# Optimization experiments

Hardware: AMD Instinct MI355X
Metric: run time of the kernel (lower is better)

Reference implementation:

```python
import jax, jax.numpy as jnp
import numpy as np

B, S, D, H = 2, 2048, 1024, 16
DK = D // H


def setup_inputs() -> dict:
    key = jax.random.key(0)
    ks = jax.random.split(key, 12)
    q = jax.random.normal(ks[0], (B, S, D), dtype=jnp.float32)
    k = jax.random.normal(ks[1], (B, S, D), dtype=jnp.float32)
    v = jax.random.normal(ks[2], (B, S, D), dtype=jnp.float32)
    # causal mask: positions where mask == 0 are masked out
    mask = jnp.tril(jnp.ones((S, S), dtype=jnp.int32))[None, None, :, :]
    s = 1.0 / np.sqrt(D)
    Wq = jax.random.uniform(ks[3], (D, D), jnp.float32, -s, s)
    bq = jax.random.uniform(ks[4], (D,), jnp.float32, -s, s)
    Wk = jax.random.uniform(ks[5], (D, D), jnp.float32, -s, s)
    bk = jax.random.uniform(ks[6], (D,), jnp.float32, -s, s)
    Wv = jax.random.uniform(ks[7], (D, D), jnp.float32, -s, s)
    bv = jax.random.uniform(ks[8], (D,), jnp.float32, -s, s)
    Wo = jax.random.uniform(ks[9], (D, D), jnp.float32, -s, s)
    bo = jax.random.uniform(ks[10], (D,), jnp.float32, -s, s)
    return {"q": q, "k": k, "v": v, "mask": mask,
            "Wq": Wq, "bq": bq, "Wk": Wk, "bk": bk,
            "Wv": Wv, "bv": bv, "Wo": Wo, "bo": bo}


def reference(q, k, v, mask, Wq, bq, Wk, bk, Wv, bv, Wo, bo):
    b = q.shape[0]
    # linear projections (nn.Linear: x @ W.T + b), split into heads -> [b,h,s,dk]
    qh = (q @ Wq.T + bq).reshape(b, -1, H, DK).transpose(0, 2, 1, 3)
    kh = (k @ Wk.T + bk).reshape(b, -1, H, DK).transpose(0, 2, 1, 3)
    vh = (v @ Wv.T + bv).reshape(b, -1, H, DK).transpose(0, 2, 1, 3)
    scores = jnp.einsum('bhqd,bhkd->bhqk', qh, kh) / jnp.sqrt(jnp.float32(DK))
    scores = jnp.where(mask == 0, jnp.float32(-1e9), scores)
    attn = jax.nn.softmax(scores, axis=-1)  # dropout p=0.0 -> identity
    out = jnp.einsum('bhqk,bhkd->bhqd', attn, vh)
    out = out.transpose(0, 2, 1, 3).reshape(b, -1, D)
    return out @ Wo.T + bo
```

## Files before the change

kernel.cpp:

```cpp
#include <hip/hip_runtime.h>


typedef _Float16 f16;
typedef __attribute__((ext_vector_type(4))) float   f32x4;
typedef __attribute__((ext_vector_type(8))) _Float16 f16x8;

#define DEVI __device__ __forceinline__

static constexpr int S  = 2048;
static constexpr int D  = 1024;
static constexpr int KK = 1024;
static constexpr int M  = 4096;

DEVI void gload_lds16(const void* g, void* l) {
  __builtin_amdgcn_global_load_lds((const __attribute__((address_space(1))) void*)g,
                                   (__attribute__((address_space(3))) void*)l, 16, 0, 0);
}

DEVI f32x4 mfma16(f16x8 a, f16x8 b, f32x4 c) {
  return __builtin_amdgcn_mfma_f32_16x16x32_f16(a, b, c, 0, 0, 0);
}

DEVI int xorv(int row) { return ((row ^ (row >> 3)) & 7) << 4; }

__global__ __launch_bounds__(256) void cvt_kernel(const float* __restrict__ s0,
                                                  const float* __restrict__ s1,
                                                  const float* __restrict__ s2,
                                                  const float* __restrict__ s3,
                                                  f16* __restrict__ dst, int nper) {
  const float* s = blockIdx.y == 0 ? s0 : blockIdx.y == 1 ? s1 : blockIdx.y == 2 ? s2 : s3;
  f16* d = dst + (size_t)blockIdx.y * nper;
  const int i = (blockIdx.x * 256 + threadIdx.x) * 8;
  f32x4 a = *(const f32x4*)(s + i);
  f32x4 b = *(const f32x4*)(s + i + 4);
  f16x8 r;
#pragma unroll
  for (int j = 0; j < 4; ++j) { r[j] = (f16)a[j]; r[4 + j] = (f16)b[j]; }
  *(f16x8*)(d + i) = r;
}

DEVI void gemm_mainloop(const f16* __restrict__ A, const f16* __restrict__ W,
                        int m0, int n0, f16* As, f16* Bs, f32x4 acc[4][4]) {
  const int tid  = threadIdx.x;
  const int wid  = tid >> 6;
  const int lane = tid & 63;
  const int wr = wid >> 1, wc = wid & 1;

  const f32x4 z4 = {0.f, 0.f, 0.f, 0.f};
#pragma unroll
  for (int mi = 0; mi < 4; ++mi)
#pragma unroll
    for (int ni = 0; ni < 4; ++ni) acc[mi][ni] = z4;

  const int r0 = tid >> 2, c0 = (tid & 3) * 8;
  const int r1 = 64 + r0;
  const f16* Ag0 = A + (size_t)(m0 + r0) * KK + c0;
  const f16* Ag1 = A + (size_t)(m0 + r1) * KK + c0;
  const f16* Bg0 = W + (size_t)(n0 + r0) * KK + c0;
  const f16* Bg1 = W + (size_t)(n0 + r1) * KK + c0;
  f16* As0 = As + wid * 512;
  f16* As1 = As + 2048 + wid * 512;
  f16* Bs0 = Bs + wid * 512;
  f16* Bs1 = Bs + 2048 + wid * 512;

  const int arow = wr * 64 + (lane & 15);
  const int brow = wc * 64 + (lane & 15);
  const int ko   = (lane >> 4) * 8;

  for (int k0 = 0; k0 < KK; k0 += 32) {
    gload_lds16(Ag0 + k0, As0);
    gload_lds16(Ag1 + k0, As1);
    gload_lds16(Bg0 + k0, Bs0);
    gload_lds16(Bg1 + k0, Bs1);
    __syncthreads();
    f16x8 af[4], bf[4];
#pragma unroll
    for (int mi = 0; mi < 4; ++mi) af[mi] = *(const f16x8*)&As[(arow + mi * 16) * 32 + ko];
#pragma unroll
    for (int ni = 0; ni < 4; ++ni) bf[ni] = *(const f16x8*)&Bs[(brow + ni * 16) * 32 + ko];
#pragma unroll
    for (int mi = 0; mi < 4; ++mi)
#pragma unroll
      for (int ni = 0; ni < 4; ++ni)
        acc[mi][ni] = mfma16(af[mi], bf[ni], acc[mi][ni]);
    __syncthreads();
  }
}

__global__ __launch_bounds__(256, 2) void gemm_qkv_kernel(const f16* __restrict__ X,
                                                          const f16* __restrict__ Wp,
                                                          const float* __restrict__ b0,
                                                          const float* __restrict__ b1,
                                                          const float* __restrict__ b2,
                                                          f16* __restrict__ Hd) {
  __shared__ f16 As[128 * 32];
  __shared__ f16 Bs[128 * 32];
  const int z = blockIdx.z;
  const f16* A = X + (size_t)z * (M * KK);
  const f16* W = Wp + (size_t)z * (D * KK);
  const float* bias = z == 0 ? b0 : z == 1 ? b1 : b2;
  f16* dst = Hd + (size_t)z * (size_t)4194304;
  const float scale = (z == 0) ? 0.125f : 1.0f;
  const int m0 = blockIdx.y * 128, n0 = blockIdx.x * 128;

  f32x4 acc[4][4];
  gemm_mainloop(A, W, m0, n0, As, Bs, acc);

  const int lane = threadIdx.x & 63, wid = threadIdx.x >> 6;
  const int wr = wid >> 1, wc = wid & 1;
#pragma unroll
  for (int ni = 0; ni < 4; ++ni) {
    const int col = n0 + wc * 64 + ni * 16 + (lane & 15);
    const float bv = bias[col];
    const int h = col >> 6, dk = col & 63;
#pragma unroll
    for (int mi = 0; mi < 4; ++mi) {
#pragma unroll
      for (int r = 0; r < 4; ++r) {
        const int row = m0 + wr * 64 + mi * 16 + (lane >> 4) * 4 + r;
        const int bb = row >> 11, ss = row & 2047;
        dst[(size_t)((bb * 16 + h) * 2048 + ss) * 64 + dk] = (f16)((acc[mi][ni][r] + bv) * scale);
      }
    }
  }
}

__global__ __launch_bounds__(256, 2) void gemm_out_kernel(const f16* __restrict__ A,
                                                          const f16* __restrict__ W,
                                                          const float* __restrict__ bias,
                                                          float* __restrict__ out) {
  __shared__ f16 As[128 * 32];
  __shared__ f16 Bs[128 * 32];
  const int m0 = blockIdx.y * 128, n0 = blockIdx.x * 128;
  f32x4 acc[4][4];
  gemm_mainloop(A, W, m0, n0, As, Bs, acc);
  const int lane = threadIdx.x & 63, wid = threadIdx.x >> 6;
  const int wr = wid >> 1, wc = wid & 1;
#pragma unroll
  for (int ni = 0; ni < 4; ++ni) {
    const int col = n0 + wc * 64 + ni * 16 + (lane & 15);
    const float bv = bias[col];
#pragma unroll
    for (int mi = 0; mi < 4; ++mi) {
#pragma unroll
      for (int r = 0; r < 4; ++r) {
        const int row = m0 + wr * 64 + mi * 16 + (lane >> 4) * 4 + r;
        out[(size_t)row * 1024 + col] = acc[mi][ni][r] + bv;
      }
    }
  }
}

__global__ __launch_bounds__(256) void vtr_kernel(const f16* __restrict__ Vh,
                                                  f16* __restrict__ VhT) {
  __shared__ f16 T[64][72];
  const int bh = blockIdx.y;
  const int s0 = blockIdx.x * 64;
  const size_t base = (size_t)bh * (S * 64);
  const int tid = threadIdx.x;
#pragma unroll
  for (int i = 0; i < 2; ++i) {
    const int c = i * 256 + tid;
    const int sr = c >> 3, sc = (c & 7) * 8;
    f16x8 v = *(const f16x8*)&Vh[base + (size_t)(s0 + sr) * 64 + sc];
    *(f16x8*)&T[sr][sc] = v;
  }
  __syncthreads();
#pragma unroll
  for (int i = 0; i < 2; ++i) {
    const int c = i * 256 + tid;
    const int dk = c >> 3, so = (c & 7) * 8;
    f16x8 r;
#pragma unroll
    for (int j = 0; j < 8; ++j) r[j] = T[so + j][dk];
    *(f16x8*)&VhT[base + (size_t)dk * S + s0 + so] = r;
  }
}

__global__ __launch_bounds__(256, 2) void attn_kernel(const f16* __restrict__ Qh,
                                                      const f16* __restrict__ Kh,
                                                      const f16* __restrict__ VhT,
                                                      f16* __restrict__ Ao) {
  __shared__ f16 Ks[2][64 * 64];
  __shared__ f16 Vt[2][64 * 64];
  __shared__ f16 Ps[4][32 * 64];

  const int tid = threadIdx.x, wid = tid >> 6, lane = tid & 63;
  const int bh = blockIdx.y;
  const int q0 = (15 - (int)blockIdx.x) * 128;
  const int qw = q0 + wid * 32;
  const size_t base = (size_t)bh * (S * 64);

  const int srow0 = tid >> 3;
  const int scol0 = (((tid & 7) * 16) ^ xorv(srow0)) >> 1;
  const int srow1 = (256 + tid) >> 3;
  const int scol1 = (((tid & 7) * 16) ^ xorv(srow1)) >> 1;
  const int ldsoff0 = wid * 64 * 16;
  const int ldsoff1 = (256 + wid * 64) * 16;

  f16x8 aq[2][2];
#pragma unroll
  for (int mi = 0; mi < 2; ++mi)
#pragma unroll
    for (int ks = 0; ks < 2; ++ks)
      aq[mi][ks] = *(const f16x8*)&Qh[base + (size_t)(qw + mi * 16 + (lane & 15)) * 64 +
                                      ks * 32 + (lane >> 4) * 8];

  const f32x4 z4 = {0.f, 0.f, 0.f, 0.f};
  f32x4 o[2][4];
  float mrow[2][4], lrow[2][4];
#pragma unroll
  for (int mi = 0; mi < 2; ++mi)
#pragma unroll
    for (int r = 0; r < 4; ++r) { mrow[mi][r] = -1e30f; lrow[mi][r] = 0.f; }
#pragma unroll
  for (int mi = 0; mi < 2; ++mi)
#pragma unroll
    for (int dj = 0; dj < 4; ++dj) o[mi][dj] = z4;

  const int ntiles = q0 / 64 + 2;

  {
    const int kv0 = 0;
    gload_lds16(Kh + base + (size_t)(kv0 + srow0) * 64 + scol0, (char*)Ks[0] + ldsoff0);
    gload_lds16(VhT + base + (size_t)srow0 * S + kv0 + scol0,   (char*)Vt[0] + ldsoff0);
    gload_lds16(Kh + base + (size_t)(kv0 + srow1) * 64 + scol1, (char*)Ks[0] + ldsoff1);
    gload_lds16(VhT + base + (size_t)srow1 * S + kv0 + scol1,   (char*)Vt[0] + ldsoff1);
  }

  int cur = 0;
  for (int t = 0; t < ntiles; ++t) {
    const int kv0 = t * 64;
    if (t + 1 < ntiles) {
      const int kn = kv0 + 64;
      f16* Kd = Ks[cur ^ 1];
      f16* Vd = Vt[cur ^ 1];
      gload_lds16(Kh + base + (size_t)(kn + srow0) * 64 + scol0, (char*)Kd + ldsoff0);
      gload_lds16(VhT + base + (size_t)srow0 * S + kn + scol0,   (char*)Vd + ldsoff0);
      gload_lds16(Kh + base + (size_t)(kn + srow1) * 64 + scol1, (char*)Kd + ldsoff1);
      gload_lds16(VhT + base + (size_t)srow1 * S + kn + scol1,   (char*)Vd + ldsoff1);
      asm volatile("s_waitcnt vmcnt(4)" ::: "memory");
    } else {
      asm volatile("s_waitcnt vmcnt(0)" ::: "memory");
    }
    __builtin_amdgcn_sched_barrier(0);
    __builtin_amdgcn_s_barrier();
    __builtin_amdgcn_sched_barrier(0);

    const f16* Kc = Ks[cur];
    const f16* Vc = Vt[cur];

    if (kv0 <= qw + 31) {
      f32x4 sc[2][4];
#pragma unroll
      for (int mi = 0; mi < 2; ++mi)
#pragma unroll
        for (int nj = 0; nj < 4; ++nj) sc[mi][nj] = z4;
      __builtin_amdgcn_s_setprio(1);
#pragma unroll
      for (int nj = 0; nj < 4; ++nj) {
        const int krow = nj * 16 + (lane & 15);
#pragma unroll
        for (int ks = 0; ks < 2; ++ks) {
          f16x8 bk = *(const f16x8*)((const char*)Kc + krow * 128 +
                                     ((ks * 64 + (lane >> 4) * 16) ^ xorv(krow)));
          sc[0][nj] = mfma16(aq[0][ks], bk, sc[0][nj]);
          sc[1][nj] = mfma16(aq[1][ks], bk, sc[1][nj]);
        }
      }
      __builtin_amdgcn_s_setprio(0);
      if (kv0 + 63 > qw) {
#pragma unroll
        for (int mi = 0; mi < 2; ++mi)
#pragma unroll
          for (int nj = 0; nj < 4; ++nj)
#pragma unroll
            for (int r = 0; r < 4; ++r) {
              const int qq = qw + mi * 16 + (lane >> 4) * 4 + r;
              const int kv = kv0 + nj * 16 + (lane & 15);
              if (kv > qq) sc[mi][nj][r] = -1e30f;
            }
      }
      float mnew[2][4], scl[2][4], psum[2][4];
#pragma unroll
      for (int mi = 0; mi < 2; ++mi)
#pragma unroll
        for (int r = 0; r < 4; ++r) {
          float mx = fmaxf(fmaxf(sc[mi][0][r], sc[mi][1][r]), fmaxf(sc[mi][2][r], sc[mi][3][r]));
#pragma unroll
          for (int off = 1; off < 16; off <<= 1) mx = fmaxf(mx, __shfl_xor(mx, off));
          const float mn = fmaxf(mrow[mi][r], mx);
          mnew[mi][r] = mn;
          scl[mi][r]  = exp2f((mrow[mi][r] - mn) * 1.44269504f);
          psum[mi][r] = 0.f;
        }
#pragma unroll
      for (int mi = 0; mi < 2; ++mi)
#pragma unroll
        for (int nj = 0; nj < 4; ++nj) {
#pragma unroll
          for (int r = 0; r < 4; ++r) {
            const float p = exp2f((sc[mi][nj][r] - mnew[mi][r]) * 1.44269504f);
            psum[mi][r] += p;
            const int ql = mi * 16 + (lane >> 4) * 4 + r;
            const int kvl = nj * 16 + (lane & 15);
            *(f16*)((char*)Ps[wid] + ql * 128 + ((kvl * 2) ^ xorv(ql))) = (f16)p;
          }
        }
#pragma unroll
      for (int mi = 0; mi < 2; ++mi)
#pragma unroll
        for (int r = 0; r < 4; ++r) {
          float ps = psum[mi][r];
#pragma unroll
          for (int off = 1; off < 16; off <<= 1) ps += __shfl_xor(ps, off);
          lrow[mi][r] = lrow[mi][r] * scl[mi][r] + ps;
          mrow[mi][r] = mnew[mi][r];
        }
#pragma unroll
      for (int mi = 0; mi < 2; ++mi)
#pragma unroll
        for (int dj = 0; dj < 4; ++dj)
#pragma unroll
          for (int r = 0; r < 4; ++r) o[mi][dj][r] *= scl[mi][r];
      __builtin_amdgcn_s_setprio(1);
#pragma unroll
      for (int ks = 0; ks < 2; ++ks) {
        f16x8 pa[2];
#pragma unroll
        for (int mi = 0; mi < 2; ++mi) {
          const int ql = mi * 16 + (lane & 15);
          pa[mi] = *(const f16x8*)((char*)Ps[wid] + ql * 128 +
                                   ((ks * 64 + (lane >> 4) * 16) ^ xorv(ql)));
        }
#pragma unroll
        for (int dj = 0; dj < 4; ++dj) {
          const int dr = dj * 16 + (lane & 15);
          f16x8 bv = *(const f16x8*)((const char*)Vc + dr * 128 +
                                     ((ks * 64 + (lane >> 4) * 16) ^ xorv(dr)));
          o[0][dj] = mfma16(pa[0], bv, o[0][dj]);
          o[1][dj] = mfma16(pa[1], bv, o[1][dj]);
        }
      }
      __builtin_amdgcn_s_setprio(0);
    }

    __builtin_amdgcn_sched_barrier(0);
    __builtin_amdgcn_s_barrier();
    cur ^= 1;
  }

  const int bb = bh >> 4, hh = bh & 15;
#pragma unroll
  for (int mi = 0; mi < 2; ++mi)
#pragma unroll
    for (int r = 0; r < 4; ++r) {
      const float inv = 1.0f / lrow[mi][r];
      const int qq = qw + mi * 16 + (lane >> 4) * 4 + r;
#pragma unroll
      for (int dj = 0; dj < 4; ++dj) {
        const int dk = dj * 16 + (lane & 15);
        Ao[(size_t)(bb * 2048 + qq) * 1024 + hh * 64 + dk] = (f16)(o[mi][dj][r] * inv);
      }
    }
}

extern "C" void kernel_launch(void* const* d_in, const int* in_sizes, int n_in,
                              void* d_out, int out_size, void* d_ws, size_t ws_size,
                              hipStream_t stream) {
  const float* q  = (const float*)d_in[0];
  const float* k  = (const float*)d_in[1];
  const float* v  = (const float*)d_in[2];
  const float* Wq = (const float*)d_in[4];  const float* bq = (const float*)d_in[5];
  const float* Wk = (const float*)d_in[6];  const float* bk = (const float*)d_in[7];
  const float* Wv = (const float*)d_in[8];  const float* bv = (const float*)d_in[9];
  const float* Wo = (const float*)d_in[10]; const float* bo = (const float*)d_in[11];
  float* out = (float*)d_out;

  char* ws = (char*)d_ws;
  f16* xb = (f16*)(ws);
  f16* wb = (f16*)(ws + 25165824);
  f16* hb = (f16*)(ws + 33554432);
  f16* ao = (f16*)(ws + 58720256);
  f16* vt = (f16*)(ws);

  cvt_kernel<<<dim3(2048, 3), 256, 0, stream>>>(q, k, v, nullptr, xb, 4194304);
  cvt_kernel<<<dim3(512, 4), 256, 0, stream>>>(Wq, Wk, Wv, Wo, wb, 1048576);
  gemm_qkv_kernel<<<dim3(8, 32, 3), 256, 0, stream>>>(xb, wb, bq, bk, bv, hb);
  vtr_kernel<<<dim3(32, 32), 256, 0, stream>>>(hb + 8388608, vt);
  attn_kernel<<<dim3(16, 32), 256, 0, stream>>>(hb, hb + 4194304, vt, ao);
  gemm_out_kernel<<<dim3(8, 32), 256, 0, stream>>>(ao, wb + 3 * 1048576, bo, out);
}
```

Before: 319.6 us.

## Split attention KV range across two blocks and merge with combine kernel

Each query block's causal KV range is split into two halves handled by separate blocks (grid z=2), so twice as many blocks run and per-block work is more balanced. Each half writes an unnormalized fp16 partial output plus running max and sum, and a new combine kernel rescales and merges the two halves into the final attention output. Launch bounds are raised to 3 blocks per SM to fit more occupancy. The cost is extra global traffic for the partials, an extra kernel launch, and fp16 storage of unnormalized accumulators, which could lose precision or overflow.

```diff
diff --git a/kernel.cpp b/kernel.cpp
--- a/kernel.cpp
+++ b/kernel.cpp
@@ -177,19 +177,24 @@
   }
 }
 
-__global__ __launch_bounds__(256, 2) void attn_kernel(const f16* __restrict__ Qh,
+__global__ __launch_bounds__(256, 3) void attn_kernel(const f16* __restrict__ Qh,
                                                       const f16* __restrict__ Kh,
                                                       const f16* __restrict__ VhT,
-                                                      f16* __restrict__ Ao) {
+                                                      f16* __restrict__ pO,
+                                                      float2* __restrict__ ml) {
   __shared__ f16 Ks[2][64 * 64];
   __shared__ f16 Vt[2][64 * 64];
   __shared__ f16 Ps[4][32 * 64];
 
   const int tid = threadIdx.x, wid = tid >> 6, lane = tid & 63;
   const int bh = blockIdx.y;
+  const int z  = blockIdx.z;
   const int q0 = (15 - (int)blockIdx.x) * 128;
   const int qw = q0 + wid * 32;
   const size_t base = (size_t)bh * (S * 64);
+
+  const int half = q0 / 128 + 1;
+  const int t0 = z * half, t1 = t0 + half;
 
   const int srow0 = tid >> 3;
   const int scol0 = (((tid & 7) * 16) ^ xorv(srow0)) >> 1;
@@ -218,10 +223,8 @@
 #pragma unroll
     for (int dj = 0; dj < 4; ++dj) o[mi][dj] = z4;
 
-  const int ntiles = q0 / 64 + 2;
-
   {
-    const int kv0 = 0;
+    const int kv0 = t0 * 64;
     gload_lds16(Kh + base + (size_t)(kv0 + srow0) * 64 + scol0, (char*)Ks[0] + ldsoff0);
     gload_lds16(VhT + base + (size_t)srow0 * S + kv0 + scol0,   (char*)Vt[0] + ldsoff0);
     gload_lds16(Kh + base + (size_t)(kv0 + srow1) * 64 + scol1, (char*)Ks[0] + ldsoff1);
@@ -229,9 +232,9 @@
   }
 
   int cur = 0;
-  for (int t = 0; t < ntiles; ++t) {
+  for (int t = t0; t < t1; ++t) {
     const int kv0 = t * 64;
-    if (t + 1 < ntiles) {
+    if (t + 1 < t1) {
       const int kn = kv0 + 64;
       f16* Kd = Ks[cur ^ 1];
       f16* Vd = Vt[cur ^ 1];
@@ -297,7 +300,7 @@
 #pragma unroll
       for (int mi = 0; mi < 2; ++mi)
 #pragma unroll
-        for (int nj = 0; nj < 4; ++nj) {
+      for (int nj = 0; nj < 4; ++nj) {
 #pragma unroll
           for (int r = 0; r < 4; ++r) {
             const float p = exp2f((sc[mi][nj][r] - mnew[mi][r]) * 1.44269504f);
@@ -350,19 +353,52 @@
     cur ^= 1;
   }
 
-  const int bb = bh >> 4, hh = bh & 15;
+  f16* po = pO + (size_t)z * 4194304 + (size_t)bh * 2048 * 64;
 #pragma unroll
   for (int mi = 0; mi < 2; ++mi)
 #pragma unroll
     for (int r = 0; r < 4; ++r) {
-      const float inv = 1.0f / lrow[mi][r];
       const int qq = qw + mi * 16 + (lane >> 4) * 4 + r;
 #pragma unroll
       for (int dj = 0; dj < 4; ++dj) {
         const int dk = dj * 16 + (lane & 15);
-        Ao[(size_t)(bb * 2048 + qq) * 1024 + hh * 64 + dk] = (f16)(o[mi][dj][r] * inv);
+        po[(size_t)qq * 64 + dk] = (f16)o[mi][dj][r];
+      }
+      if ((lane & 15) == 0) {
+        float2 v; v.x = mrow[mi][r]; v.y = lrow[mi][r];
+        ml[(size_t)z * 65536 + bh * 2048 + qq] = v;
       }
     }
+}
+
+__global__ __launch_bounds__(256) void comb_kernel(const f16* __restrict__ pO,
+                                                   const float2* __restrict__ ml,
+                                                   f16* __restrict__ Ao) {
+  const int gid = blockIdx.x * 256 + threadIdx.x;
+  const int rid = gid >> 2;
+  const int c0  = (gid & 3) * 16;
+  const float2 a = ml[rid];
+  const float2 b = ml[65536 + rid];
+  const float m  = fmaxf(a.x, b.x);
+  const float e0 = exp2f((a.x - m) * 1.44269504f);
+  const float e1 = exp2f((b.x - m) * 1.44269504f);
+  const float inv = 1.0f / (a.y * e0 + b.y * e1);
+  const float s0 = e0 * inv, s1 = e1 * inv;
+  const f16* p0 = pO + (size_t)rid * 64 + c0;
+  const f16* p1 = p0 + 4194304;
+  f16x8 x0 = *(const f16x8*)p0, x1 = *(const f16x8*)(p0 + 8);
+  f16x8 y0 = *(const f16x8*)p1, y1 = *(const f16x8*)(p1 + 8);
+  f16x8 r0, r1;
+#pragma unroll
+  for (int j = 0; j < 8; ++j) {
+    r0[j] = (f16)((float)x0[j] * s0 + (float)y0[j] * s1);
+    r1[j] = (f16)((float)x1[j] * s0 + (float)y1[j] * s1);
+  }
+  const int bh = rid >> 11, ss = rid & 2047;
+  const int bb = bh >> 4, hh = bh & 15;
+  f16* dst = Ao + (size_t)(bb * 2048 + ss) * 1024 + hh * 64 + c0;
+  *(f16x8*)dst = r0;
+  *(f16x8*)(dst + 8) = r1;
 }
 
 extern "C" void kernel_launch(void* const* d_in, const int* in_sizes, int n_in,
@@ -383,11 +419,14 @@
   f16* hb = (f16*)(ws + 33554432);
   f16* ao = (f16*)(ws + 58720256);
   f16* vt = (f16*)(ws);
+  f16* po = (f16*)(ws + 8388608);
+  float2* mlp = (float2*)(ws + 50331648);
 
   cvt_kernel<<<dim3(2048, 3), 256, 0, stream>>>(q, k, v, nullptr, xb, 4194304);
   cvt_kernel<<<dim3(512, 4), 256, 0, stream>>>(Wq, Wk, Wv, Wo, wb, 1048576);
   gemm_qkv_kernel<<<dim3(8, 32, 3), 256, 0, stream>>>(xb, wb, bq, bk, bv, hb);
   vtr_kernel<<<dim3(32, 32), 256, 0, stream>>>(hb + 8388608, vt);
-  attn_kernel<<<dim3(16, 32), 256, 0, stream>>>(hb, hb + 4194304, vt, ao);
+  attn_kernel<<<dim3(16, 32, 2), 256, 0, stream>>>(hb, hb + 4194304, vt, po, mlp);
+  comb_kernel<<<1024, 256, 0, stream>>>(po, mlp, ao);
   gemm_out_kernel<<<dim3(8, 32), 256, 0, stream>>>(ao, wb + 3 * 1048576, bo, out);
 }
```

Result: slower. 386.2 us (+20.8%).
